# Optimization experiments

Measured on AMD Instinct MI355X. Metric: run time of the kernel, lower is better.

Reference implementation:

```python
import jax, jax.numpy as jnp
from jax import lax
import numpy as np


def _gru_cell(x, h, wih, whh, bih, bhh):
    # torch.nn.GRUCell math: gates split order (r, z, n)
    gi = x @ wih.T + bih          # (N, 3H)
    gh = h @ whh.T + bhh          # (N, 3H)
    ir, iz, i_n = jnp.split(gi, 3, axis=-1)
    hr, hz, h_n = jnp.split(gh, 3, axis=-1)
    r = jax.nn.sigmoid(ir + hr)
    z = jax.nn.sigmoid(iz + hz)
    n = jnp.tanh(i_n + r * h_n)
    return (1.0 - z) * n + z * h


def _dilated_gru(x, dilation, wih, whh, bih, bhh):
    # h_i depends on h_{i-dilation} -> `dilation` independent chains,
    # scanned jointly with a carried state of shape (B*dilation, H).
    B, S, I = x.shape
    H = whh.shape[1]
    nc = S // dilation  # assumes S % dilation == 0
    xr = x.reshape(B, nc, dilation, I).transpose(1, 0, 2, 3).reshape(nc, B * dilation, I)

    def step(h, xt):
        hn = _gru_cell(xt, h, wih, whh, bih, bhh)
        return hn, hn

    h0 = jnp.zeros((B * dilation, H), x.dtype)
    _, ys = lax.scan(step, h0, xr)  # (nc, B*dilation, H)
    return ys.reshape(nc, B, dilation, H).transpose(1, 0, 2, 3).reshape(B, S, H)


def _encoder(data, fparams, bparams, dilations):
    outs = []
    x = data
    for p, d in zip(fparams, dilations):
        x = _dilated_gru(x, d, *p)
        outs.append(x[:, -1, :])
    x = data[:, ::-1, :]
    for p, d in zip(bparams, dilations):
        x = _dilated_gru(x, d, *p)
        outs.append(x[:, -1, :])
    return jnp.concatenate(outs, axis=1)  # (B, 2*sum(hidden_sizes)) = (B, 400)


def setup_inputs() -> dict:
    key = jax.random.key(0)
    ks = jax.random.split(key, 7)
    B, S = 1024, 512
    sizes = [(1, 100), (100, 50), (50, 50)]  # (input_size, hidden_size) per layer

    def cell(k, iS, H):
        k1, k2, k3, k4 = jax.random.split(k, 4)
        s = 1.0 / np.sqrt(H)  # torch GRUCell init: U(-1/sqrt(H), 1/sqrt(H))
        u = lambda kk, shp: jax.random.uniform(kk, shp, jnp.float32, -s, s)
        return u(k1, (3 * H, iS)), u(k2, (3 * H, H)), u(k3, (3 * H,)), u(k4, (3 * H,))

    d = {"data": jax.random.normal(ks[0], (B, S, 1), jnp.float32)}
    for i, nm in enumerate(["f1", "f2", "f3", "b1", "b2", "b3"]):
        iS, H = sizes[i % 3]
        w1, w2, bb1, bb2 = cell(ks[i + 1], iS, H)
        d[nm + "_wih"] = w1
        d[nm + "_whh"] = w2
        d[nm + "_bih"] = bb1
        d[nm + "_bhh"] = bb2
    return d


def reference(data,
              f1_wih, f1_whh, f1_bih, f1_bhh,
              f2_wih, f2_whh, f2_bih, f2_bhh,
              f3_wih, f3_whh, f3_bih, f3_bhh,
              b1_wih, b1_whh, b1_bih, b1_bhh,
              b2_wih, b2_whh, b2_bih, b2_bhh,
              b3_wih, b3_whh, b3_bih, b3_bhh):
    dilations = (1, 4, 16)
    fparams = [(f1_wih, f1_whh, f1_bih, f1_bhh),
               (f2_wih, f2_whh, f2_bih, f2_bhh),
               (f3_wih, f3_whh, f3_bih, f3_bhh)]
    bparams = [(b1_wih, b1_whh, b1_bih, b1_bhh),
               (b2_wih, b2_whh, b2_bih, b2_bhh),
               (b3_wih, b3_whh, b3_bih, b3_bhh)]
    return _encoder(data, fparams, bparams, dilations)
```

## Files before the change

### kernel.cpp

```cpp
#include <hip/hip_runtime.h>
#include <math.h>

typedef short  s16x8 __attribute__((ext_vector_type(8)));
typedef float  f32x4 __attribute__((ext_vector_type(4)));

static __device__ __forceinline__ float sigf(float x){ return 1.0f/(1.0f+__expf(-x)); }
static __device__ __forceinline__ float tanhf_fast(float x){
  float ax=fabsf(x); float e=__expf(-2.0f*ax); float t=(1.0f-e)/(1.0f+e); return copysignf(t,x);
}
static __device__ __forceinline__ unsigned short f2bf(float x){
  unsigned int u = __float_as_uint(x);
  unsigned int r = (u + 0x7FFFu + ((u >> 16) & 1u)) >> 16;
  return (unsigned short)r;
}
static __device__ __forceinline__ float bf2f(unsigned short b){
  return __uint_as_float(((unsigned int)b) << 16);
}
static __device__ __forceinline__ float qsum(float v){
  v += __int_as_float(__builtin_amdgcn_mov_dpp(__float_as_int(v),0xB1,0xF,0xF,true));
  v += __int_as_float(__builtin_amdgcn_mov_dpp(__float_as_int(v),0x4E,0xF,0xF,true));
  return v;
}
static __device__ __forceinline__ float rsum4(float v){
  return v + __int_as_float(__builtin_amdgcn_ds_swizzle(__float_as_int(v), 0x101F));
}
static __device__ __forceinline__ float sel4(int c, float4 v){
  float r=v.x; r=(c==1)?v.y:r; r=(c==2)?v.z:r; r=(c==3)?v.w:r; return r;
}

static __device__ __forceinline__ void load_afrag(const float* __restrict__ whh,
                                                  int gate, int ti, int l, int kc,
                                                  s16x8& hi, s16x8& lo){
  const int r  = ti*16 + (l & 15);
  const int kb = kc*32 + (l >> 4)*8;
  #pragma unroll
  for (int j = 0; j < 8; ++j){
    const int k = kb + j;
    const float wv = (r < 100 && k < 100) ? whh[(size_t)(gate*100 + r)*100 + k] : 0.0f;
    const unsigned short hb = f2bf(wv);
    hi[j] = (short)hb;
    lo[j] = (short)f2bf(wv - bf2f(hb));
  }
}

__global__ __launch_bounds__(448, 2)
void gru_l1(const float* __restrict__ data,
            const float* __restrict__ wih_f, const float* __restrict__ whh_f,
            const float* __restrict__ bih_f, const float* __restrict__ bhh_f,
            const float* __restrict__ wih_b, const float* __restrict__ whh_b,
            const float* __restrict__ bih_b, const float* __restrict__ bhh_b,
            float* __restrict__ x1f, float* __restrict__ x1b,
            float* __restrict__ out)
{
  const int dir   = (int)(blockIdx.x >> 6);
  const int blk16 = (int)(blockIdx.x & 63);
  const int t     = (int)threadIdx.x;
  const float* __restrict__ wih = dir ? wih_b : wih_f;
  const float* __restrict__ whh = dir ? whh_b : whh_f;
  const float* __restrict__ bih = dir ? bih_b : bih_f;
  const float* __restrict__ bhh = dir ? bhh_b : bhh_f;
  float* __restrict__ x1 = dir ? x1b : x1f;
  const int obase = dir ? 200 : 0;
  const int b0 = blk16 * 16;

  __shared__ __align__(16) unsigned short hBhi[2][16][136];
  __shared__ __align__(16) unsigned short hBlo[2][16][136];
  __shared__ __align__(16) float xs[512][16];

  for (int i = t; i < 8192; i += 448){
    const int c  = i >> 9;
    const int sL = i & 511;
    xs[sL][c] = data[(size_t)(b0 + c)*512 + (size_t)(dir ? (511 - sL) : sL)];
  }
  { unsigned short* ph = (unsigned short*)hBhi;
    unsigned short* pl = (unsigned short*)hBlo;
    for (int i = t; i < 2*16*136; i += 448){ ph[i] = 0; pl[i] = 0; } }

  const int l  = t & 63;
  const int W  = t >> 6;

  s16x8 AH00,AH01,AH02,AH03, AH10,AH11,AH12,AH13, AH20,AH21,AH22,AH23;
  s16x8 AL00,AL01,AL02,AL03, AL10,AL11,AL12,AL13, AL20,AL21,AL22,AL23;
  #define LDA(G,KC) load_afrag(whh, G, W, l, KC, AH##G##KC, AL##G##KC);
  LDA(0,0) LDA(0,1) LDA(0,2) LDA(0,3)
  LDA(1,0) LDA(1,1) LDA(1,2) LDA(1,3)
  LDA(2,0) LDA(2,1) LDA(2,2) LDA(2,3)
  #undef LDA

  const int mg  = (l >> 4) * 4;
  const int u0  = W*16 + mg;
  const bool uvalid = (u0 < 100);
  const int u0c = uvalid ? u0 : 96;
  const int c   = l & 15;
  const f32x4 wxr4 = *(const f32x4*)&wih[u0c];
  const f32x4 wxz4 = *(const f32x4*)&wih[100 + u0c];
  const f32x4 wxn4 = *(const f32x4*)&wih[200 + u0c];
  const f32x4 bcr4 = *(const f32x4*)&bih[u0c]       + *(const f32x4*)&bhh[u0c];
  const f32x4 bcz4 = *(const f32x4*)&bih[100 + u0c] + *(const f32x4*)&bhh[100 + u0c];
  const f32x4 bxn4 = *(const f32x4*)&bih[200 + u0c];
  const f32x4 bhn4 = *(const f32x4*)&bhh[200 + u0c];
  f32x4 hprev = {0.f,0.f,0.f,0.f};

  __syncthreads();

  const int bn = l & 15;
  const int bg = (l >> 4)*8;

  #pragma unroll 1
  for (int s = 0; s < 512; ++s){
    const int cur = s & 1, nxt = cur ^ 1;

    const s16x8 BH0 = *(const s16x8*)&hBhi[cur][bn][ 0 + bg];
    const s16x8 BL0 = *(const s16x8*)&hBlo[cur][bn][ 0 + bg];
    const s16x8 BH1 = *(const s16x8*)&hBhi[cur][bn][32 + bg];
    const s16x8 BL1 = *(const s16x8*)&hBlo[cur][bn][32 + bg];
    const s16x8 BH2 = *(const s16x8*)&hBhi[cur][bn][64 + bg];
    const s16x8 BL2 = *(const s16x8*)&hBlo[cur][bn][64 + bg];
    const s16x8 BH3 = *(const s16x8*)&hBhi[cur][bn][96 + bg];
    const s16x8 BL3 = *(const s16x8*)&hBlo[cur][bn][96 + bg];

    f32x4 Ca0={0.f,0.f,0.f,0.f}, Cb0={0.f,0.f,0.f,0.f};
    f32x4 Ca1={0.f,0.f,0.f,0.f}, Cb1={0.f,0.f,0.f,0.f};
    f32x4 Ca2={0.f,0.f,0.f,0.f}, Cb2={0.f,0.f,0.f,0.f};
    #define MM(ACC,G,KC) \
      ACC = __builtin_amdgcn_mfma_f32_16x16x32_bf16(AL##G##KC, BH##KC, ACC, 0, 0, 0); \
      ACC = __builtin_amdgcn_mfma_f32_16x16x32_bf16(AH##G##KC, BL##KC, ACC, 0, 0, 0); \
      ACC = __builtin_amdgcn_mfma_f32_16x16x32_bf16(AH##G##KC, BH##KC, ACC, 0, 0, 0);
    MM(Ca0,0,0) MM(Ca1,1,0) MM(Ca2,2,0)
    MM(Cb0,0,2) MM(Cb1,1,2) MM(Cb2,2,2)
    MM(Ca0,0,1) MM(Ca1,1,1) MM(Ca2,2,1)
    MM(Cb0,0,3) MM(Cb1,1,3) MM(Cb2,2,3)
    #undef MM
    const f32x4 sr = Ca0 + Cb0;
    const f32x4 sz = Ca1 + Cb1;
    const f32x4 sn = Ca2 + Cb2;

    const float xc = xs[s][c];
    f32x4 hn;
    #define FIN(I) { \
      const float rr = sigf(sr[I] + fmaf(wxr4[I], xc, bcr4[I])); \
      const float zz = sigf(sz[I] + fmaf(wxz4[I], xc, bcz4[I])); \
      const float nn = tanhf_fast(fmaf(wxn4[I], xc, bxn4[I]) + rr*(sn[I] + bhn4[I])); \
      hn[I] = nn + zz*(hprev[I] - nn); }
    FIN(0) FIN(1) FIN(2) FIN(3)
    #undef FIN
    hprev = hn;

    if (uvalid){
      const unsigned short h0 = f2bf(hn[0]), h1 = f2bf(hn[1]), h2 = f2bf(hn[2]), h3 = f2bf(hn[3]);
      uint2 vhi, vlo;
      vhi.x = (unsigned int)h0 | ((unsigned int)h1 << 16);
      vhi.y = (unsigned int)h2 | ((unsigned int)h3 << 16);
      vlo.x = (unsigned int)f2bf(hn[0] - bf2f(h0)) | ((unsigned int)f2bf(hn[1] - bf2f(h1)) << 16);
      vlo.y = (unsigned int)f2bf(hn[2] - bf2f(h2)) | ((unsigned int)f2bf(hn[3] - bf2f(h3)) << 16);
      *(uint2*)&hBhi[nxt][c][u0] = vhi;
      *(uint2*)&hBlo[nxt][c][u0] = vlo;
      if ((s & 3) == 3){
        const int cs = s >> 2;
        const int ch = b0 + c;
        const size_t base = (((size_t)cs*256 + (ch >> 2))*100);
        x1[(base + u0 + 0)*4 + (ch & 3)] = hn[0];
        x1[(base + u0 + 1)*4 + (ch & 3)] = hn[1];
        x1[(base + u0 + 2)*4 + (ch & 3)] = hn[2];
        x1[(base + u0 + 3)*4 + (ch & 3)] = hn[3];
      }
      if (s == 511){
        const int ch = b0 + c;
        *(f32x4*)&out[(size_t)ch*400 + obase + u0] = hn;
      }
    }
    __syncthreads();
  }
}

__global__ __launch_bounds__(512, 4)
void gru_l2(const float* __restrict__ x1f, const float* __restrict__ x1b,
            const float* __restrict__ wih_f, const float* __restrict__ whh_f,
            const float* __restrict__ bih_f, const float* __restrict__ bhh_f,
            const float* __restrict__ wih_b, const float* __restrict__ whh_b,
            const float* __restrict__ bih_b, const float* __restrict__ bhh_b,
            float* __restrict__ x2f, float* __restrict__ x2b,
            float* __restrict__ out)
{
  const int dir = (int)(blockIdx.x >> 8);
  const int blk = (int)(blockIdx.x & 255);
  const int t   = (int)threadIdx.x;
  const float* __restrict__ wih = dir ? wih_b : wih_f;
  const float* __restrict__ whh = dir ? whh_b : whh_f;
  const float* __restrict__ bih = dir ? bih_b : bih_f;
  const float* __restrict__ bhh = dir ? bhh_b : bhh_f;
  const float* __restrict__ x1 = dir ? x1b : x1f;
  float* __restrict__ x2 = dir ? x2b : x2f;
  const int obase = dir ? 300 : 100;
  const int b0 = blk * 4;

  __shared__ __align__(16) float xh[2][152][4];

  const int oct = t >> 3;
  const int u   = (oct > 49) ? 49 : oct;
  const int l   = t & 7;
  const int cb  = 19 * l;
  float4 W0,W1,W2,W3,W4,W5,W6,W7,W8,W9,W10,W11,W12,W13,W14,W15,W16,W17,W18;
  #define L2LW(J, V) { const int g = cb + (J); \
    const float wr_ = (g<100) ? wih[(size_t)(u     )*100+g] : ((g<150)? whh[(size_t)(u     )*50+g-100] : 0.f); \
    const float wz_ = (g<100) ? wih[(size_t)(u + 50)*100+g] : ((g<150)? whh[(size_t)(u + 50)*50+g-100] : 0.f); \
    const float wx_ = (g<100) ? wih[(size_t)(u +100)*100+g] : 0.f; \
    const float wh_ = (g>=100 && g<150) ? whh[(size_t)(u +100)*50+g-100] : 0.f; \
    V = make_float4(wr_, wz_, wx_, wh_); }
  L2LW(0,W0)  L2LW(1,W1)  L2LW(2,W2)  L2LW(3,W3)  L2LW(4,W4)  L2LW(5,W5)  L2LW(6,W6)
  L2LW(7,W7)  L2LW(8,W8)  L2LW(9,W9)  L2LW(10,W10) L2LW(11,W11) L2LW(12,W12) L2LW(13,W13)
  L2LW(14,W14) L2LW(15,W15) L2LW(16,W16) L2LW(17,W17) L2LW(18,W18)
  #undef L2LW
  const float bcr = bih[u] + bhh[u];
  const float bcz = bih[u+50] + bhh[u+50];
  const float bxn = bih[u+100];
  const float bhn = bhh[u+100];

  for (int i = t; i < 104; i += 512){
    const int bi = (i >= 52) ? 1 : 0;
    const int row = 100 + (i - bi*52);
    *(float4*)&xh[bi][row][0] = make_float4(0.f,0.f,0.f,0.f);
  }
  if (t < 100)
    *(float4*)&xh[0][t][0] = *(const float4*)(x1 + (((size_t)0*256 + blk)*100 + t)*4);
  __syncthreads();

  #pragma unroll 1
  for (int s = 0; s < 128; ++s){
    const int cur = s & 1, nxt = cur ^ 1;
    if (t < 400){
      const float* hb = &xh[cur][cb][0];
      float ar0=0,ar1=0,ar2=0,ar3=0, az0=0,az1=0,az2=0,az3=0;
      float ax0=0,ax1=0,ax2=0,ax3=0, ah0=0,ah1=0,ah2=0,ah3=0;
      #define L2C(J, WV) { const float4 h4 = *(const float4*)(hb + 4*(J)); \
        ar0=fmaf(WV.x,h4.x,ar0); ar1=fmaf(WV.x,h4.y,ar1); ar2=fmaf(WV.x,h4.z,ar2); ar3=fmaf(WV.x,h4.w,ar3); \
        az0=fmaf(WV.y,h4.x,az0); az1=fmaf(WV.y,h4.y,az1); az2=fmaf(WV.y,h4.z,az2); az3=fmaf(WV.y,h4.w,az3); \
        ax0=fmaf(WV.z,h4.x,ax0); ax1=fmaf(WV.z,h4.y,ax1); ax2=fmaf(WV.z,h4.z,ax2); ax3=fmaf(WV.z,h4.w,ax3); \
        ah0=fmaf(WV.w,h4.x,ah0); ah1=fmaf(WV.w,h4.y,ah1); ah2=fmaf(WV.w,h4.z,ah2); ah3=fmaf(WV.w,h4.w,ah3); }
      L2C(0,W0)  L2C(1,W1)  L2C(2,W2)  L2C(3,W3)  L2C(4,W4)  L2C(5,W5)  L2C(6,W6)
      L2C(7,W7)  L2C(8,W8)  L2C(9,W9)  L2C(10,W10) L2C(11,W11) L2C(12,W12) L2C(13,W13)
      L2C(14,W14) L2C(15,W15) L2C(16,W16) L2C(17,W17) L2C(18,W18)
      #undef L2C
      ar0=qsum(ar0); ar1=qsum(ar1); ar2=qsum(ar2); ar3=qsum(ar3);
      az0=qsum(az0); az1=qsum(az1); az2=qsum(az2); az3=qsum(az3);
      ax0=qsum(ax0); ax1=qsum(ax1); ax2=qsum(ax2); ax3=qsum(ax3);
      ah0=qsum(ah0); ah1=qsum(ah1); ah2=qsum(ah2); ah3=qsum(ah3);
      ar0=rsum4(ar0); ar1=rsum4(ar1); ar2=rsum4(ar2); ar3=rsum4(ar3);
      az0=rsum4(az0); az1=rsum4(az1); az2=rsum4(az2); az3=rsum4(az3);
      ax0=rsum4(ax0); ax1=rsum4(ax1); ax2=rsum4(ax2); ax3=rsum4(ax3);
      ah0=rsum4(ah0); ah1=rsum4(ah1); ah2=rsum4(ah2); ah3=rsum4(ah3);
      if (l < 4){
        const float Ar = sel4(l, make_float4(ar0,ar1,ar2,ar3));
        const float Az = sel4(l, make_float4(az0,az1,az2,az3));
        const float Ax = sel4(l, make_float4(ax0,ax1,ax2,ax3));
        const float Ah = sel4(l, make_float4(ah0,ah1,ah2,ah3));
        const float ho = xh[cur][100+u][l];
        const float r = sigf(Ar + bcr);
        const float z = sigf(Az + bcz);
        const float n = tanhf_fast(Ax + bxn + r*(Ah + bhn));
        const float hnew = n + z*(ho - n);
        xh[nxt][100+u][l] = hnew;
        if ((s & 3) == 3) x2[(((size_t)(s>>2)*256 + blk)*50 + u)*4 + l] = hnew;
        if (s == 127)     out[(size_t)(b0 + l)*400 + obase + u] = hnew;
      }
    } else if (t < 500){
      if (s + 1 < 128){
        const int j = t - 400;
        *(float4*)&xh[nxt][j][0] = *(const float4*)(x1 + (((size_t)(s+1)*256 + blk)*100 + j)*4);
      }
    }
    __syncthreads();
  }
}

__global__ __launch_bounds__(512, 4)
void gru_l3(const float* __restrict__ x2f, const float* __restrict__ x2b,
            const float* __restrict__ wih_f, const float* __restrict__ whh_f,
            const float* __restrict__ bih_f, const float* __restrict__ bhh_f,
            const float* __restrict__ wih_b, const float* __restrict__ whh_b,
            const float* __restrict__ bih_b, const float* __restrict__ bhh_b,
            float* __restrict__ out)
{
  const int dir = (int)(blockIdx.x >> 8);
  const int blk = (int)(blockIdx.x & 255);
  const int t   = (int)threadIdx.x;
  const float* __restrict__ wih = dir ? wih_b : wih_f;
  const float* __restrict__ whh = dir ? whh_b : whh_f;
  const float* __restrict__ bih = dir ? bih_b : bih_f;
  const float* __restrict__ bhh = dir ? bhh_b : bhh_f;
  const float* __restrict__ x2 = dir ? x2b : x2f;
  const int obase = dir ? 350 : 150;
  const int b0 = blk * 4;

  __shared__ __align__(16) float xh[2][104][4];

  const int oct = t >> 3;
  const int u   = (oct > 49) ? 49 : oct;
  const int l   = t & 7;
  const int cb  = 13 * l;
  float4 W0,W1,W2,W3,W4,W5,W6,W7,W8,W9,W10,W11,W12;
  #define L3LW(J, V) { const int g = cb + (J); \
    const float wr_ = (g<50) ? wih[(size_t)(u     )*50+g] : ((g<100)? whh[(size_t)(u     )*50+g-50] : 0.f); \
    const float wz_ = (g<50) ? wih[(size_t)(u + 50)*50+g] : ((g<100)? whh[(size_t)(u + 50)*50+g-50] : 0.f); \
    const float wx_ = (g<50) ? wih[(size_t)(u +100)*50+g] : 0.f; \
    const float wh_ = (g>=50 && g<100) ? whh[(size_t)(u +100)*50+g-50] : 0.f; \
    V = make_float4(wr_, wz_, wx_, wh_); }
  L3LW(0,W0) L3LW(1,W1) L3LW(2,W2) L3LW(3,W3) L3LW(4,W4) L3LW(5,W5) L3LW(6,W6)
  L3LW(7,W7) L3LW(8,W8) L3LW(9,W9) L3LW(10,W10) L3LW(11,W11) L3LW(12,W12)
  #undef L3LW
  const float bcr = bih[u] + bhh[u];
  const float bcz = bih[u+50] + bhh[u+50];
  const float bxn = bih[u+100];
  const float bhn = bhh[u+100];

  for (int i = t; i < 108; i += 512){
    const int bi = (i >= 54) ? 1 : 0;
    const int row = 50 + (i - bi*54);
    *(float4*)&xh[bi][row][0] = make_float4(0.f,0.f,0.f,0.f);
  }
  if (t < 50)
    *(float4*)&xh[0][t][0] = *(const float4*)(x2 + (((size_t)0*256 + blk)*50 + t)*4);
  __syncthreads();

  #pragma unroll 1
  for (int s = 0; s < 32; ++s){
    const int cur = s & 1, nxt = cur ^ 1;
    if (t < 400){
      const float* hb = &xh[cur][cb][0];
      float ar0=0,ar1=0,ar2=0,ar3=0, az0=0,az1=0,az2=0,az3=0;
      float ax0=0,ax1=0,ax2=0,ax3=0, ah0=0,ah1=0,ah2=0,ah3=0;
      #define L3C(J, WV) { const float4 h4 = *(const float4*)(hb + 4*(J)); \
        ar0=fmaf(WV.x,h4.x,ar0); ar1=fmaf(WV.x,h4.y,ar1); ar2=fmaf(WV.x,h4.z,ar2); ar3=fmaf(WV.x,h4.w,ar3); \
        az0=fmaf(WV.y,h4.x,az0); az1=fmaf(WV.y,h4.y,az1); az2=fmaf(WV.y,h4.z,az2); az3=fmaf(WV.y,h4.w,az3); \
        ax0=fmaf(WV.z,h4.x,ax0); ax1=fmaf(WV.z,h4.y,ax1); ax2=fmaf(WV.z,h4.z,ax2); ax3=fmaf(WV.z,h4.w,ax3); \
        ah0=fmaf(WV.w,h4.x,ah0); ah1=fmaf(WV.w,h4.y,ah1); ah2=fmaf(WV.w,h4.z,ah2); ah3=fmaf(WV.w,h4.w,ah3); }
      L3C(0,W0) L3C(1,W1) L3C(2,W2) L3C(3,W3) L3C(4,W4) L3C(5,W5) L3C(6,W6)
      L3C(7,W7) L3C(8,W8) L3C(9,W9) L3C(10,W10) L3C(11,W11) L3C(12,W12)
      #undef L3C
      ar0=qsum(ar0); ar1=qsum(ar1); ar2=qsum(ar2); ar3=qsum(ar3);
      az0=qsum(az0); az1=qsum(az1); az2=qsum(az2); az3=qsum(az3);
      ax0=qsum(ax0); ax1=qsum(ax1); ax2=qsum(ax2); ax3=qsum(ax3);
      ah0=qsum(ah0); ah1=qsum(ah1); ah2=qsum(ah2); ah3=qsum(ah3);
      ar0=rsum4(ar0); ar1=rsum4(ar1); ar2=rsum4(ar2); ar3=rsum4(ar3);
      az0=rsum4(az0); az1=rsum4(az1); az2=rsum4(az2); az3=rsum4(az3);
      ax0=rsum4(ax0); ax1=rsum4(ax1); ax2=rsum4(ax2); ax3=rsum4(ax3);
      ah0=rsum4(ah0); ah1=rsum4(ah1); ah2=rsum4(ah2); ah3=rsum4(ah3);
      if (l < 4){
        const float Ar = sel4(l, make_float4(ar0,ar1,ar2,ar3));
        const float Az = sel4(l, make_float4(az0,az1,az2,az3));
        const float Ax = sel4(l, make_float4(ax0,ax1,ax2,ax3));
        const float Ah = sel4(l, make_float4(ah0,ah1,ah2,ah3));
        const float ho = xh[cur][50+u][l];
        const float r = sigf(Ar + bcr);
        const float z = sigf(Az + bcz);
        const float n = tanhf_fast(Ax + bxn + r*(Ah + bhn));
        const float hnew = n + z*(ho - n);
        xh[nxt][50+u][l] = hnew;
        if (s == 31) out[(size_t)(b0 + l)*400 + obase + u] = hnew;
      }
    } else if (t < 450){
      if (s + 1 < 32){
        const int j = t - 400;
        *(float4*)&xh[nxt][j][0] = *(const float4*)(x2 + (((size_t)(s+1)*256 + blk)*50 + j)*4);
      }
    }
    __syncthreads();
  }
}

extern "C" void kernel_launch(void* const* d_in, const int* in_sizes, int n_in,
                              void* d_out, int out_size, void* d_ws, size_t ws_size,
                              hipStream_t stream)
{
  const float* data   = (const float*)d_in[0];
  const float* f1_wih = (const float*)d_in[1];
  const float* f1_whh = (const float*)d_in[2];
  const float* f1_bih = (const float*)d_in[3];
  const float* f1_bhh = (const float*)d_in[4];
  const float* f2_wih = (const float*)d_in[5];
  const float* f2_whh = (const float*)d_in[6];
  const float* f2_bih = (const float*)d_in[7];
  const float* f2_bhh = (const float*)d_in[8];
  const float* f3_wih = (const float*)d_in[9];
  const float* f3_whh = (const float*)d_in[10];
  const float* f3_bih = (const float*)d_in[11];
  const float* f3_bhh = (const float*)d_in[12];
  const float* b1_wih = (const float*)d_in[13];
  const float* b1_whh = (const float*)d_in[14];
  const float* b1_bih = (const float*)d_in[15];
  const float* b1_bhh = (const float*)d_in[16];
  const float* b2_wih = (const float*)d_in[17];
  const float* b2_whh = (const float*)d_in[18];
  const float* b2_bih = (const float*)d_in[19];
  const float* b2_bhh = (const float*)d_in[20];
  const float* b3_wih = (const float*)d_in[21];
  const float* b3_whh = (const float*)d_in[22];
  const float* b3_bih = (const float*)d_in[23];
  const float* b3_bhh = (const float*)d_in[24];
  float* out = (float*)d_out;

  const size_t X1N = (size_t)128 * 256 * 100 * 4;
  const size_t X2N = (size_t)32 * 256 * 50 * 4;
  if (ws_size < (2 * X1N + 2 * X2N) * sizeof(float)) return;
  float* wsf = (float*)d_ws;
  float* x1f = wsf;
  float* x1b = wsf + X1N;
  float* x2f = wsf + 2 * X1N;
  float* x2b = wsf + 2 * X1N + X2N;

  gru_l1<<<dim3(128), dim3(448), 0, stream>>>(
      data, f1_wih, f1_whh, f1_bih, f1_bhh,
      b1_wih, b1_whh, b1_bih, b1_bhh, x1f, x1b, out);
  gru_l2<<<dim3(512), dim3(512), 0, stream>>>(
      x1f, x1b, f2_wih, f2_whh, f2_bih, f2_bhh,
      b2_wih, b2_whh, b2_bih, b2_bhh, x2f, x2b, out);
  gru_l3<<<dim3(512), dim3(512), 0, stream>>>(
      x2f, x2b, f3_wih, f3_whh, f3_bih, f3_bhh,
      b3_wih, b3_whh, b3_bih, b3_bhh, out);
}
```

Baseline: 1.185 ms.

## Give each wave two hidden tiles in layer-1 GRU, shrink block to four waves

The layer-1 recurrent kernel now runs 4 waves per block, each owning two 16-row output tiles instead of one, so fewer waves join the per-step barrier and more MFMA work runs between barriers. The hidden-state split into bf16 hi/lo now uses the packed v_cvt_pk_bf16_f32 instruction instead of manual rounding. Output pointers are precomputed and advanced per chunk, and the loop is unrolled by two. The cost is roughly double the A-fragment register footprint per thread and a longer serial MFMA chain per wave on the critical recurrence path.

```diff
diff --git a/kernel.cpp b/kernel.cpp
--- a/kernel.cpp
+++ b/kernel.cpp
@@ -16,6 +16,11 @@
 static __device__ __forceinline__ float bf2f(unsigned short b){
   return __uint_as_float(((unsigned int)b) << 16);
 }
+static __device__ __forceinline__ unsigned int cvt_pk_bf16(float a, float b){
+  unsigned int r;
+  asm("v_cvt_pk_bf16_f32 %0, %1, %2" : "=v"(r) : "v"(a), "v"(b));
+  return r;
+}
 static __device__ __forceinline__ float qsum(float v){
   v += __int_as_float(__builtin_amdgcn_mov_dpp(__float_as_int(v),0xB1,0xF,0xF,true));
   v += __int_as_float(__builtin_amdgcn_mov_dpp(__float_as_int(v),0x4E,0xF,0xF,true));
@@ -29,9 +34,9 @@
 }
 
 static __device__ __forceinline__ void load_afrag(const float* __restrict__ whh,
-                                                  int gate, int ti, int l, int kc,
+                                                  int gate, int tile, int l, int kc,
                                                   s16x8& hi, s16x8& lo){
-  const int r  = ti*16 + (l & 15);
+  const int r  = tile*16 + (l & 15);
   const int kb = kc*32 + (l >> 4)*8;
   #pragma unroll
   for (int j = 0; j < 8; ++j){
@@ -43,7 +48,7 @@
   }
 }
 
-__global__ __launch_bounds__(448, 2)
+__global__ __launch_bounds__(256, 1)
 void gru_l1(const float* __restrict__ data,
             const float* __restrict__ wih_f, const float* __restrict__ whh_f,
             const float* __restrict__ bih_f, const float* __restrict__ bhh_f,
@@ -67,48 +72,71 @@
   __shared__ __align__(16) unsigned short hBlo[2][16][136];
   __shared__ __align__(16) float xs[512][16];
 
-  for (int i = t; i < 8192; i += 448){
+  for (int i = t; i < 8192; i += 256){
     const int c  = i >> 9;
     const int sL = i & 511;
     xs[sL][c] = data[(size_t)(b0 + c)*512 + (size_t)(dir ? (511 - sL) : sL)];
   }
   { unsigned short* ph = (unsigned short*)hBhi;
     unsigned short* pl = (unsigned short*)hBlo;
-    for (int i = t; i < 2*16*136; i += 448){ ph[i] = 0; pl[i] = 0; } }
+    for (int i = t; i < 2*16*136; i += 256){ ph[i] = 0; pl[i] = 0; } }
 
   const int l  = t & 63;
   const int W  = t >> 6;
-
-  s16x8 AH00,AH01,AH02,AH03, AH10,AH11,AH12,AH13, AH20,AH21,AH22,AH23;
-  s16x8 AL00,AL01,AL02,AL03, AL10,AL11,AL12,AL13, AL20,AL21,AL22,AL23;
-  #define LDA(G,KC) load_afrag(whh, G, W, l, KC, AH##G##KC, AL##G##KC);
-  LDA(0,0) LDA(0,1) LDA(0,2) LDA(0,3)
-  LDA(1,0) LDA(1,1) LDA(1,2) LDA(1,3)
-  LDA(2,0) LDA(2,1) LDA(2,2) LDA(2,3)
+  const int tA = 2*W, tB = 2*W + 1;
+
+  #define DECLA(G,T) s16x8 AH##G##T##0, AH##G##T##1, AH##G##T##2, AH##G##T##3, \
+                           AL##G##T##0, AL##G##T##1, AL##G##T##2, AL##G##T##3;
+  DECLA(0,a) DECLA(1,a) DECLA(2,a) DECLA(0,b) DECLA(1,b) DECLA(2,b)
+  #undef DECLA
+  #define LDA(G,T,TI) \
+    load_afrag(whh, G, TI, l, 0, AH##G##T##0, AL##G##T##0); \
+    load_afrag(whh, G, TI, l, 1, AH##G##T##1, AL##G##T##1); \
+    load_afrag(whh, G, TI, l, 2, AH##G##T##2, AL##G##T##2); \
+    load_afrag(whh, G, TI, l, 3, AH##G##T##3, AL##G##T##3);
+  LDA(0,a,tA) LDA(1,a,tA) LDA(2,a,tA)
+  LDA(0,b,tB) LDA(1,b,tB) LDA(2,b,tB)
   #undef LDA
 
   const int mg  = (l >> 4) * 4;
-  const int u0  = W*16 + mg;
-  const bool uvalid = (u0 < 100);
-  const int u0c = uvalid ? u0 : 96;
   const int c   = l & 15;
-  const f32x4 wxr4 = *(const f32x4*)&wih[u0c];
-  const f32x4 wxz4 = *(const f32x4*)&wih[100 + u0c];
-  const f32x4 wxn4 = *(const f32x4*)&wih[200 + u0c];
-  const f32x4 bcr4 = *(const f32x4*)&bih[u0c]       + *(const f32x4*)&bhh[u0c];
-  const f32x4 bcz4 = *(const f32x4*)&bih[100 + u0c] + *(const f32x4*)&bhh[100 + u0c];
-  const f32x4 bxn4 = *(const f32x4*)&bih[200 + u0c];
-  const f32x4 bhn4 = *(const f32x4*)&bhh[200 + u0c];
-  f32x4 hprev = {0.f,0.f,0.f,0.f};
+  const int uA0 = tA*16 + mg;
+  const int uB0 = tB*16 + mg;
+  const bool vA = (uA0 < 100);
+  const bool vB = (uB0 < 100);
+  const int uA = vA ? uA0 : 96;
+  const int uB = vB ? uB0 : 96;
+  const f32x4 wxrA = *(const f32x4*)&wih[uA];
+  const f32x4 wxzA = *(const f32x4*)&wih[100 + uA];
+  const f32x4 wxnA = *(const f32x4*)&wih[200 + uA];
+  const f32x4 bcrA = *(const f32x4*)&bih[uA]       + *(const f32x4*)&bhh[uA];
+  const f32x4 bczA = *(const f32x4*)&bih[100 + uA] + *(const f32x4*)&bhh[100 + uA];
+  const f32x4 bxnA = *(const f32x4*)&bih[200 + uA];
+  const f32x4 bhnA = *(const f32x4*)&bhh[200 + uA];
+  const f32x4 wxrB = *(const f32x4*)&wih[uB];
+  const f32x4 wxzB = *(const f32x4*)&wih[100 + uB];
+  const f32x4 wxnB = *(const f32x4*)&wih[200 + uB];
+  const f32x4 bcrB = *(const f32x4*)&bih[uB]       + *(const f32x4*)&bhh[uB];
+  const f32x4 bczB = *(const f32x4*)&bih[100 + uB] + *(const f32x4*)&bhh[100 + uB];
+  const f32x4 bxnB = *(const f32x4*)&bih[200 + uB];
+  const f32x4 bhnB = *(const f32x4*)&bhh[200 + uB];
+  f32x4 hpA = {0.f,0.f,0.f,0.f};
+  f32x4 hpB = {0.f,0.f,0.f,0.f};
+
+  const int ch = b0 + c;
+  float* pA = x1 + ((size_t)(ch >> 2)*100 + uA0)*4 + (ch & 3);
+  float* pB = x1 + ((size_t)(ch >> 2)*100 + uB0)*4 + (ch & 3);
+  const size_t CSSTRIDE = (size_t)256*100*4;
 
   __syncthreads();
 
-  const int bn = l & 15;
+  const int bn = c;
   const int bg = (l >> 4)*8;
 
-  #pragma unroll 1
+  #pragma unroll 2
   for (int s = 0; s < 512; ++s){
     const int cur = s & 1, nxt = cur ^ 1;
+    const float xc = xs[s][c];
 
     const s16x8 BH0 = *(const s16x8*)&hBhi[cur][bn][ 0 + bg];
     const s16x8 BL0 = *(const s16x8*)&hBlo[cur][bn][ 0 + bg];
@@ -119,55 +147,72 @@
     const s16x8 BH3 = *(const s16x8*)&hBhi[cur][bn][96 + bg];
     const s16x8 BL3 = *(const s16x8*)&hBlo[cur][bn][96 + bg];
 
-    f32x4 Ca0={0.f,0.f,0.f,0.f}, Cb0={0.f,0.f,0.f,0.f};
-    f32x4 Ca1={0.f,0.f,0.f,0.f}, Cb1={0.f,0.f,0.f,0.f};
-    f32x4 Ca2={0.f,0.f,0.f,0.f}, Cb2={0.f,0.f,0.f,0.f};
-    #define MM(ACC,G,KC) \
-      ACC = __builtin_amdgcn_mfma_f32_16x16x32_bf16(AL##G##KC, BH##KC, ACC, 0, 0, 0); \
-      ACC = __builtin_amdgcn_mfma_f32_16x16x32_bf16(AH##G##KC, BL##KC, ACC, 0, 0, 0); \
-      ACC = __builtin_amdgcn_mfma_f32_16x16x32_bf16(AH##G##KC, BH##KC, ACC, 0, 0, 0);
-    MM(Ca0,0,0) MM(Ca1,1,0) MM(Ca2,2,0)
-    MM(Cb0,0,2) MM(Cb1,1,2) MM(Cb2,2,2)
-    MM(Ca0,0,1) MM(Ca1,1,1) MM(Ca2,2,1)
-    MM(Cb0,0,3) MM(Cb1,1,3) MM(Cb2,2,3)
-    #undef MM
-    const f32x4 sr = Ca0 + Cb0;
-    const f32x4 sz = Ca1 + Cb1;
-    const f32x4 sn = Ca2 + Cb2;
-
-    const float xc = xs[s][c];
-    f32x4 hn;
-    #define FIN(I) { \
-      const float rr = sigf(sr[I] + fmaf(wxr4[I], xc, bcr4[I])); \
-      const float zz = sigf(sz[I] + fmaf(wxz4[I], xc, bcz4[I])); \
-      const float nn = tanhf_fast(fmaf(wxn4[I], xc, bxn4[I]) + rr*(sn[I] + bhn4[I])); \
-      hn[I] = nn + zz*(hprev[I] - nn); }
-    FIN(0) FIN(1) FIN(2) FIN(3)
+    f32x4 C0a={0.f,0.f,0.f,0.f}, C1a={0.f,0.f,0.f,0.f}, C2a={0.f,0.f,0.f,0.f};
+    f32x4 C0b={0.f,0.f,0.f,0.f}, C1b={0.f,0.f,0.f,0.f}, C2b={0.f,0.f,0.f,0.f};
+    #define MM3(ACC,AH,AL,BH,BL) \
+      ACC = __builtin_amdgcn_mfma_f32_16x16x32_bf16(AL, BH, ACC, 0, 0, 0); \
+      ACC = __builtin_amdgcn_mfma_f32_16x16x32_bf16(AH, BL, ACC, 0, 0, 0); \
+      ACC = __builtin_amdgcn_mfma_f32_16x16x32_bf16(AH, BH, ACC, 0, 0, 0);
+    #define MMKC(KC) \
+      MM3(C0a, AH0a##KC, AL0a##KC, BH##KC, BL##KC) \
+      MM3(C1a, AH1a##KC, AL1a##KC, BH##KC, BL##KC) \
+      MM3(C2a, AH2a##KC, AL2a##KC, BH##KC, BL##KC) \
+      MM3(C0b, AH0b##KC, AL0b##KC, BH##KC, BL##KC) \
+      MM3(C1b, AH1b##KC, AL1b##KC, BH##KC, BL##KC) \
+      MM3(C2b, AH2b##KC, AL2b##KC, BH##KC, BL##KC)
+    MMKC(0) MMKC(1) MMKC(2) MMKC(3)
+    #undef MMKC
+    #undef MM3
+
+    f32x4 hnA, hnB;
+    #define FIN(I,SR,SZ,SN,WXR,WXZ,WXN,BCR,BCZ,BXN,BHN,HP,HN) { \
+      const float rr = sigf(SR[I] + fmaf(WXR[I], xc, BCR[I])); \
+      const float zz = sigf(SZ[I] + fmaf(WXZ[I], xc, BCZ[I])); \
+      const float nn = tanhf_fast(fmaf(WXN[I], xc, BXN[I]) + rr*(SN[I] + BHN[I])); \
+      HN[I] = nn + zz*(HP[I] - nn); }
+    FIN(0,C0a,C1a,C2a,wxrA,wxzA,wxnA,bcrA,bczA,bxnA,bhnA,hpA,hnA)
+    FIN(1,C0a,C1a,C2a,wxrA,wxzA,wxnA,bcrA,bczA,bxnA,bhnA,hpA,hnA)
+    FIN(2,C0a,C1a,C2a,wxrA,wxzA,wxnA,bcrA,bczA,bxnA,bhnA,hpA,hnA)
+    FIN(3,C0a,C1a,C2a,wxrA,wxzA,wxnA,bcrA,bczA,bxnA,bhnA,hpA,hnA)
+    FIN(0,C0b,C1b,C2b,wxrB,wxzB,wxnB,bcrB,bczB,bxnB,bhnB,hpB,hnB)
+    FIN(1,C0b,C1b,C2b,wxrB,wxzB,wxnB,bcrB,bczB,bxnB,bhnB,hpB,hnB)
+    FIN(2,C0b,C1b,C2b,wxrB,wxzB,wxnB,bcrB,bczB,bxnB,bhnB,hpB,hnB)
+    FIN(3,C0b,C1b,C2b,wxrB,wxzB,wxnB,bcrB,bczB,bxnB,bhnB,hpB,hnB)
     #undef FIN
-    hprev = hn;
-
-    if (uvalid){
-      const unsigned short h0 = f2bf(hn[0]), h1 = f2bf(hn[1]), h2 = f2bf(hn[2]), h3 = f2bf(hn[3]);
-      uint2 vhi, vlo;
-      vhi.x = (unsigned int)h0 | ((unsigned int)h1 << 16);
-      vhi.y = (unsigned int)h2 | ((unsigned int)h3 << 16);
-      vlo.x = (unsigned int)f2bf(hn[0] - bf2f(h0)) | ((unsigned int)f2bf(hn[1] - bf2f(h1)) << 16);
-      vlo.y = (unsigned int)f2bf(hn[2] - bf2f(h2)) | ((unsigned int)f2bf(hn[3] - bf2f(h3)) << 16);
-      *(uint2*)&hBhi[nxt][c][u0] = vhi;
-      *(uint2*)&hBlo[nxt][c][u0] = vlo;
-      if ((s & 3) == 3){
-        const int cs = s >> 2;
-        const int ch = b0 + c;
-        const size_t base = (((size_t)cs*256 + (ch >> 2))*100);
-        x1[(base + u0 + 0)*4 + (ch & 3)] = hn[0];
-        x1[(base + u0 + 1)*4 + (ch & 3)] = hn[1];
-        x1[(base + u0 + 2)*4 + (ch & 3)] = hn[2];
-        x1[(base + u0 + 3)*4 + (ch & 3)] = hn[3];
-      }
-      if (s == 511){
-        const int ch = b0 + c;
-        *(f32x4*)&out[(size_t)ch*400 + obase + u0] = hn;
-      }
+    hpA = hnA; hpB = hnB;
+
+    if (vA){
+      const unsigned int px = cvt_pk_bf16(hnA[0], hnA[1]);
+      const unsigned int py = cvt_pk_bf16(hnA[2], hnA[3]);
+      const float l0 = hnA[0] - __uint_as_float(px << 16);
+      const float l1 = hnA[1] - __uint_as_float(px & 0xFFFF0000u);
+      const float l2 = hnA[2] - __uint_as_float(py << 16);
+      const float l3 = hnA[3] - __uint_as_float(py & 0xFFFF0000u);
+      uint2 vhi; vhi.x = px; vhi.y = py;
+      uint2 vlo; vlo.x = cvt_pk_bf16(l0, l1); vlo.y = cvt_pk_bf16(l2, l3);
+      *(uint2*)&hBhi[nxt][c][uA0] = vhi;
+      *(uint2*)&hBlo[nxt][c][uA0] = vlo;
+    }
+    if (vB){
+      const unsigned int px = cvt_pk_bf16(hnB[0], hnB[1]);
+      const unsigned int py = cvt_pk_bf16(hnB[2], hnB[3]);
+      const float l0 = hnB[0] - __uint_as_float(px << 16);
+      const float l1 = hnB[1] - __uint_as_float(px & 0xFFFF0000u);
+      const float l2 = hnB[2] - __uint_as_float(py << 16);
+      const float l3 = hnB[3] - __uint_as_float(py & 0xFFFF0000u);
+      uint2 vhi; vhi.x = px; vhi.y = py;
+      uint2 vlo; vlo.x = cvt_pk_bf16(l0, l1); vlo.y = cvt_pk_bf16(l2, l3);
+      *(uint2*)&hBhi[nxt][c][uB0] = vhi;
+      *(uint2*)&hBlo[nxt][c][uB0] = vlo;
+    }
+
+    if ((s & 3) == 3){
+      if (vA){ pA[0]=hnA[0]; pA[4]=hnA[1]; pA[8]=hnA[2]; pA[12]=hnA[3]; pA += CSSTRIDE; }
+      if (vB){ pB[0]=hnB[0]; pB[4]=hnB[1]; pB[8]=hnB[2]; pB[12]=hnB[3]; pB += CSSTRIDE; }
+    }
+    if (s == 511){
+      if (vA) *(f32x4*)&out[(size_t)ch*400 + obase + uA0] = hnA;
+      if (vB) *(f32x4*)&out[(size_t)ch*400 + obase + uB0] = hnB;
     }
     __syncthreads();
   }
@@ -408,7 +453,7 @@
   float* x2f = wsf + 2 * X1N;
   float* x2b = wsf + 2 * X1N + X2N;
 
-  gru_l1<<<dim3(128), dim3(448), 0, stream>>>(
+  gru_l1<<<dim3(128), dim3(256), 0, stream>>>(
       data, f1_wih, f1_whh, f1_bih, f1_bhh,
       b1_wih, b1_whh, b1_bih, b1_bhh, x1f, x1b, out);
   gru_l2<<<dim3(512), dim3(512), 0, stream>>>(
```

After: 1.223 ms. 3.2% more time.

## Rewrite layer-2 GRU as split-bf16 MFMA kernel over 16-chain tiles

Applied to the files above, without the earlier changes.

Replaces the scalar FMA/DPP-reduction layer-2 recurrence with an MFMA formulation. Each block handles 16 chains, with the concatenated [x;h] vector stored as hi/lo bf16 pairs and weights kept in register A-fragments, mirroring layer 1. It also swaps the manual bf16 rounding for packed v_cvt_pk_bf16 and replaces __syncthreads with a lighter lgkmcnt wait plus s_barrier. The grid shrinks from 512 to 128 blocks, which lowers parallelism and adds padding waste in the K dimension in exchange for matrix-core throughput.

```diff
diff --git a/kernel.cpp b/kernel.cpp
--- a/kernel.cpp
+++ b/kernel.cpp
@@ -16,6 +16,15 @@
 static __device__ __forceinline__ float bf2f(unsigned short b){
   return __uint_as_float(((unsigned int)b) << 16);
 }
+static __device__ __forceinline__ unsigned int cvt_pk_bf16(float a, float b){
+  unsigned int r;
+  asm("v_cvt_pk_bf16_f32 %0, %1, %2" : "=v"(r) : "v"(a), "v"(b));
+  return r;
+}
+static __device__ __forceinline__ void fast_barrier(){
+  asm volatile("s_waitcnt lgkmcnt(0)" ::: "memory");
+  __builtin_amdgcn_s_barrier();
+}
 static __device__ __forceinline__ float qsum(float v){
   v += __int_as_float(__builtin_amdgcn_mov_dpp(__float_as_int(v),0xB1,0xF,0xF,true));
   v += __int_as_float(__builtin_amdgcn_mov_dpp(__float_as_int(v),0x4E,0xF,0xF,true));
@@ -29,9 +38,9 @@
 }
 
 static __device__ __forceinline__ void load_afrag(const float* __restrict__ whh,
-                                                  int gate, int ti, int l, int kc,
+                                                  int gate, int tile, int l, int kc,
                                                   s16x8& hi, s16x8& lo){
-  const int r  = ti*16 + (l & 15);
+  const int r  = tile*16 + (l & 15);
   const int kb = kc*32 + (l >> 4)*8;
   #pragma unroll
   for (int j = 0; j < 8; ++j){
@@ -103,7 +112,7 @@
 
   __syncthreads();
 
-  const int bn = l & 15;
+  const int bn = c;
   const int bg = (l >> 4)*8;
 
   #pragma unroll 1
@@ -147,12 +156,14 @@
     hprev = hn;
 
     if (uvalid){
-      const unsigned short h0 = f2bf(hn[0]), h1 = f2bf(hn[1]), h2 = f2bf(hn[2]), h3 = f2bf(hn[3]);
-      uint2 vhi, vlo;
-      vhi.x = (unsigned int)h0 | ((unsigned int)h1 << 16);
-      vhi.y = (unsigned int)h2 | ((unsigned int)h3 << 16);
-      vlo.x = (unsigned int)f2bf(hn[0] - bf2f(h0)) | ((unsigned int)f2bf(hn[1] - bf2f(h1)) << 16);
-      vlo.y = (unsigned int)f2bf(hn[2] - bf2f(h2)) | ((unsigned int)f2bf(hn[3] - bf2f(h3)) << 16);
+      const unsigned int px = cvt_pk_bf16(hn[0], hn[1]);
+      const unsigned int py = cvt_pk_bf16(hn[2], hn[3]);
+      const float l0 = hn[0] - __uint_as_float(px << 16);
+      const float l1 = hn[1] - __uint_as_float(px & 0xFFFF0000u);
+      const float l2 = hn[2] - __uint_as_float(py << 16);
+      const float l3 = hn[3] - __uint_as_float(py & 0xFFFF0000u);
+      uint2 vhi; vhi.x = px; vhi.y = py;
+      uint2 vlo; vlo.x = cvt_pk_bf16(l0, l1); vlo.y = cvt_pk_bf16(l2, l3);
       *(uint2*)&hBhi[nxt][c][u0] = vhi;
       *(uint2*)&hBlo[nxt][c][u0] = vlo;
       if ((s & 3) == 3){
@@ -169,11 +180,37 @@
         *(f32x4*)&out[(size_t)ch*400 + obase + u0] = hn;
       }
     }
-    __syncthreads();
-  }
-}
-
-__global__ __launch_bounds__(512, 4)
+    fast_barrier();
+  }
+}
+
+static __device__ __forceinline__ float l2w(const float* __restrict__ wih,
+                                            const float* __restrict__ whh,
+                                            int sec, int r, int k){
+  if (r >= 50) return 0.f;
+  if (sec == 2) return (k < 100) ? wih[(size_t)(100 + r)*100 + k] : 0.f;
+  if (sec == 3) return (k >= 104 && k < 154) ? whh[(size_t)(100 + r)*50 + (k - 104)] : 0.f;
+  const int ro = (sec == 1) ? 50 : 0;
+  if (k < 100) return wih[(size_t)(ro + r)*100 + k];
+  if (k >= 104 && k < 154) return whh[(size_t)(ro + r)*50 + (k - 104)];
+  return 0.f;
+}
+static __device__ __forceinline__ void l2_afrag(const float* __restrict__ wih,
+                                                const float* __restrict__ whh,
+                                                int sec, int tile, int l, int kc,
+                                                s16x8& hi, s16x8& lo){
+  const int r  = tile*16 + (l & 15);
+  const int kb = kc*32 + (l >> 4)*8;
+  #pragma unroll
+  for (int j = 0; j < 8; ++j){
+    const float wv = l2w(wih, whh, sec, r, kb + j);
+    const unsigned short hb = f2bf(wv);
+    hi[j] = (short)hb;
+    lo[j] = (short)f2bf(wv - bf2f(hb));
+  }
+}
+
+__global__ __launch_bounds__(256, 1)
 void gru_l2(const float* __restrict__ x1f, const float* __restrict__ x1b,
             const float* __restrict__ wih_f, const float* __restrict__ whh_f,
             const float* __restrict__ bih_f, const float* __restrict__ bhh_f,
@@ -182,9 +219,9 @@
             float* __restrict__ x2f, float* __restrict__ x2b,
             float* __restrict__ out)
 {
-  const int dir = (int)(blockIdx.x >> 8);
-  const int blk = (int)(blockIdx.x & 255);
-  const int t   = (int)threadIdx.x;
+  const int dir   = (int)(blockIdx.x >> 6);
+  const int blk16 = (int)(blockIdx.x & 63);
+  const int t     = (int)threadIdx.x;
   const float* __restrict__ wih = dir ? wih_b : wih_f;
   const float* __restrict__ whh = dir ? whh_b : whh_f;
   const float* __restrict__ bih = dir ? bih_b : bih_f;
@@ -192,84 +229,173 @@
   const float* __restrict__ x1 = dir ? x1b : x1f;
   float* __restrict__ x2 = dir ? x2b : x2f;
   const int obase = dir ? 300 : 100;
-  const int b0 = blk * 4;
-
-  __shared__ __align__(16) float xh[2][152][4];
-
-  const int oct = t >> 3;
-  const int u   = (oct > 49) ? 49 : oct;
-  const int l   = t & 7;
-  const int cb  = 19 * l;
-  float4 W0,W1,W2,W3,W4,W5,W6,W7,W8,W9,W10,W11,W12,W13,W14,W15,W16,W17,W18;
-  #define L2LW(J, V) { const int g = cb + (J); \
-    const float wr_ = (g<100) ? wih[(size_t)(u     )*100+g] : ((g<150)? whh[(size_t)(u     )*50+g-100] : 0.f); \
-    const float wz_ = (g<100) ? wih[(size_t)(u + 50)*100+g] : ((g<150)? whh[(size_t)(u + 50)*50+g-100] : 0.f); \
-    const float wx_ = (g<100) ? wih[(size_t)(u +100)*100+g] : 0.f; \
-    const float wh_ = (g>=100 && g<150) ? whh[(size_t)(u +100)*50+g-100] : 0.f; \
-    V = make_float4(wr_, wz_, wx_, wh_); }
-  L2LW(0,W0)  L2LW(1,W1)  L2LW(2,W2)  L2LW(3,W3)  L2LW(4,W4)  L2LW(5,W5)  L2LW(6,W6)
-  L2LW(7,W7)  L2LW(8,W8)  L2LW(9,W9)  L2LW(10,W10) L2LW(11,W11) L2LW(12,W12) L2LW(13,W13)
-  L2LW(14,W14) L2LW(15,W15) L2LW(16,W16) L2LW(17,W17) L2LW(18,W18)
-  #undef L2LW
-  const float bcr = bih[u] + bhh[u];
-  const float bcz = bih[u+50] + bhh[u+50];
-  const float bxn = bih[u+100];
-  const float bhn = bhh[u+100];
-
-  for (int i = t; i < 104; i += 512){
-    const int bi = (i >= 52) ? 1 : 0;
-    const int row = 100 + (i - bi*52);
-    *(float4*)&xh[bi][row][0] = make_float4(0.f,0.f,0.f,0.f);
-  }
-  if (t < 100)
-    *(float4*)&xh[0][t][0] = *(const float4*)(x1 + (((size_t)0*256 + blk)*100 + t)*4);
+  const int b0 = blk16 * 16;
+
+  __shared__ __align__(16) unsigned short hBhi[2][16][168];
+  __shared__ __align__(16) unsigned short hBlo[2][16][168];
+
+  { unsigned short* ph = (unsigned short*)hBhi;
+    unsigned short* pl = (unsigned short*)hBlo;
+    for (int i = t; i < 2*16*168; i += 256){ ph[i] = 0; pl[i] = 0; } }
+
+  const int l = t & 63;
+  const int W = t >> 6;
+
+  s16x8 AH00,AH01,AH02,AH03,AH04, AH10,AH11,AH12,AH13,AH14,
+        AH20,AH21,AH22,AH23,AH24, AH30,AH31,AH32,AH33,AH34;
+  s16x8 AL00,AL01,AL02,AL03,AL04, AL10,AL11,AL12,AL13,AL14,
+        AL20,AL21,AL22,AL23,AL24, AL30,AL31,AL32,AL33,AL34;
+  #define LDA(SE,KC) l2_afrag(wih, whh, SE, W, l, KC, AH##SE##KC, AL##SE##KC);
+  LDA(0,0) LDA(0,1) LDA(0,2) LDA(0,3) LDA(0,4)
+  LDA(1,0) LDA(1,1) LDA(1,2) LDA(1,3) LDA(1,4)
+  LDA(2,0) LDA(2,1) LDA(2,2) LDA(2,3) LDA(2,4)
+  LDA(3,0) LDA(3,1) LDA(3,2) LDA(3,3) LDA(3,4)
+  #undef LDA
+
+  const int mg = (l >> 4) * 4;
+  const int c  = l & 15;
+  const int u0 = W*16 + mg;
+  const int ch = b0 + c;
+  f32x4 bcr, bcz, bxn, bhn;
+  #pragma unroll
+  for (int i = 0; i < 4; ++i){
+    const int u = (u0 + i < 50) ? (u0 + i) : 49;
+    bcr[i] = bih[u]      + bhh[u];
+    bcz[i] = bih[50 + u] + bhh[50 + u];
+    bxn[i] = bih[100 + u];
+    bhn[i] = bhh[100 + u];
+  }
+  const bool vH = (u0 < 50);
+  f32x4 hp = {0.f,0.f,0.f,0.f};
+
+  float* px = x2 + (((size_t)(ch >> 2))*50 + u0)*4 + (ch & 3);
+  const size_t X2STRIDE = (size_t)256*50*4;
+
+  const int oct  = t >> 4;
+  const int cc   = t & 15;
+  const bool stg = (t < 208);
+  const int u0x  = oct * 8;
+
   __syncthreads();
+
+  if (stg){
+    const float* p = x1 + ((size_t)0*256 + (b0 >> 2) + (cc >> 2))*400 + (cc & 3);
+    float xv[8];
+    #pragma unroll
+    for (int j = 0; j < 8; ++j){
+      const int uu = u0x + j;
+      xv[j] = (uu < 100) ? p[4*uu] : 0.f;
+    }
+    unsigned int h0 = cvt_pk_bf16(xv[0], xv[1]);
+    unsigned int h1 = cvt_pk_bf16(xv[2], xv[3]);
+    unsigned int h2 = cvt_pk_bf16(xv[4], xv[5]);
+    unsigned int h3 = cvt_pk_bf16(xv[6], xv[7]);
+    uint4 vhi; vhi.x=h0; vhi.y=h1; vhi.z=h2; vhi.w=h3;
+    uint4 vlo;
+    vlo.x = cvt_pk_bf16(xv[0]-__uint_as_float(h0<<16), xv[1]-__uint_as_float(h0&0xFFFF0000u));
+    vlo.y = cvt_pk_bf16(xv[2]-__uint_as_float(h1<<16), xv[3]-__uint_as_float(h1&0xFFFF0000u));
+    vlo.z = cvt_pk_bf16(xv[4]-__uint_as_float(h2<<16), xv[5]-__uint_as_float(h2&0xFFFF0000u));
+    vlo.w = cvt_pk_bf16(xv[6]-__uint_as_float(h3<<16), xv[7]-__uint_as_float(h3&0xFFFF0000u));
+    *(uint4*)&hBhi[0][cc][u0x] = vhi;
+    *(uint4*)&hBlo[0][cc][u0x] = vlo;
+  }
+  __syncthreads();
+
+  const int bn = c;
+  const int bg = (l >> 4)*8;
 
   #pragma unroll 1
   for (int s = 0; s < 128; ++s){
     const int cur = s & 1, nxt = cur ^ 1;
-    if (t < 400){
-      const float* hb = &xh[cur][cb][0];
-      float ar0=0,ar1=0,ar2=0,ar3=0, az0=0,az1=0,az2=0,az3=0;
-      float ax0=0,ax1=0,ax2=0,ax3=0, ah0=0,ah1=0,ah2=0,ah3=0;
-      #define L2C(J, WV) { const float4 h4 = *(const float4*)(hb + 4*(J)); \
-        ar0=fmaf(WV.x,h4.x,ar0); ar1=fmaf(WV.x,h4.y,ar1); ar2=fmaf(WV.x,h4.z,ar2); ar3=fmaf(WV.x,h4.w,ar3); \
-        az0=fmaf(WV.y,h4.x,az0); az1=fmaf(WV.y,h4.y,az1); az2=fmaf(WV.y,h4.z,az2); az3=fmaf(WV.y,h4.w,az3); \
-        ax0=fmaf(WV.z,h4.x,ax0); ax1=fmaf(WV.z,h4.y,ax1); ax2=fmaf(WV.z,h4.z,ax2); ax3=fmaf(WV.z,h4.w,ax3); \
-        ah0=fmaf(WV.w,h4.x,ah0); ah1=fmaf(WV.w,h4.y,ah1); ah2=fmaf(WV.w,h4.z,ah2); ah3=fmaf(WV.w,h4.w,ah3); }
-      L2C(0,W0)  L2C(1,W1)  L2C(2,W2)  L2C(3,W3)  L2C(4,W4)  L2C(5,W5)  L2C(6,W6)
-      L2C(7,W7)  L2C(8,W8)  L2C(9,W9)  L2C(10,W10) L2C(11,W11) L2C(12,W12) L2C(13,W13)
-      L2C(14,W14) L2C(15,W15) L2C(16,W16) L2C(17,W17) L2C(18,W18)
-      #undef L2C
-      ar0=qsum(ar0); ar1=qsum(ar1); ar2=qsum(ar2); ar3=qsum(ar3);
-      az0=qsum(az0); az1=qsum(az1); az2=qsum(az2); az3=qsum(az3);
-      ax0=qsum(ax0); ax1=qsum(ax1); ax2=qsum(ax2); ax3=qsum(ax3);
-      ah0=qsum(ah0); ah1=qsum(ah1); ah2=qsum(ah2); ah3=qsum(ah3);
-      ar0=rsum4(ar0); ar1=rsum4(ar1); ar2=rsum4(ar2); ar3=rsum4(ar3);
-      az0=rsum4(az0); az1=rsum4(az1); az2=rsum4(az2); az3=rsum4(az3);
-      ax0=rsum4(ax0); ax1=rsum4(ax1); ax2=rsum4(ax2); ax3=rsum4(ax3);
-      ah0=rsum4(ah0); ah1=rsum4(ah1); ah2=rsum4(ah2); ah3=rsum4(ah3);
-      if (l < 4){
-        const float Ar = sel4(l, make_float4(ar0,ar1,ar2,ar3));
-        const float Az = sel4(l, make_float4(az0,az1,az2,az3));
-        const float Ax = sel4(l, make_float4(ax0,ax1,ax2,ax3));
-        const float Ah = sel4(l, make_float4(ah0,ah1,ah2,ah3));
-        const float ho = xh[cur][100+u][l];
-        const float r = sigf(Ar + bcr);
-        const float z = sigf(Az + bcz);
-        const float n = tanhf_fast(Ax + bxn + r*(Ah + bhn));
-        const float hnew = n + z*(ho - n);
-        xh[nxt][100+u][l] = hnew;
-        if ((s & 3) == 3) x2[(((size_t)(s>>2)*256 + blk)*50 + u)*4 + l] = hnew;
-        if (s == 127)     out[(size_t)(b0 + l)*400 + obase + u] = hnew;
+
+    float xv0=0,xv1=0,xv2=0,xv3=0,xv4=0,xv5=0,xv6=0,xv7=0;
+    if (stg){
+      const int st = (s + 1 < 128) ? (s + 1) : 127;
+      const float* p = x1 + ((size_t)st*256 + (b0 >> 2) + (cc >> 2))*400 + (cc & 3);
+      #define XL(J, V) { const int uu = u0x + (J); \
+        V = (uu < 100) ? p[4*uu] : 0.f; }
+      XL(0,xv0) XL(1,xv1) XL(2,xv2) XL(3,xv3) XL(4,xv4) XL(5,xv5) XL(6,xv6) XL(7,xv7)
+      #undef XL
+    }
+
+    const s16x8 BH0 = *(const s16x8*)&hBhi[cur][bn][  0 + bg];
+    const s16x8 BL0 = *(const s16x8*)&hBlo[cur][bn][  0 + bg];
+    const s16x8 BH1 = *(const s16x8*)&hBhi[cur][bn][ 32 + bg];
+    const s16x8 BL1 = *(const s16x8*)&hBlo[cur][bn][ 32 + bg];
+    const s16x8 BH2 = *(const s16x8*)&hBhi[cur][bn][ 64 + bg];
+    const s16x8 BL2 = *(const s16x8*)&hBlo[cur][bn][ 64 + bg];
+    const s16x8 BH3 = *(const s16x8*)&hBhi[cur][bn][ 96 + bg];
+    const s16x8 BL3 = *(const s16x8*)&hBlo[cur][bn][ 96 + bg];
+    const s16x8 BH4 = *(const s16x8*)&hBhi[cur][bn][128 + bg];
+    const s16x8 BL4 = *(const s16x8*)&hBlo[cur][bn][128 + bg];
+
+    f32x4 CrA={0.f,0.f,0.f,0.f}, CzA={0.f,0.f,0.f,0.f}, CxA={0.f,0.f,0.f,0.f}, ChA={0.f,0.f,0.f,0.f};
+    f32x4 CrB={0.f,0.f,0.f,0.f}, CzB={0.f,0.f,0.f,0.f}, CxB={0.f,0.f,0.f,0.f}, ChB={0.f,0.f,0.f,0.f};
+    #define MF(ACC,A,B) ACC = __builtin_amdgcn_mfma_f32_16x16x32_bf16(A, B, ACC, 0, 0, 0);
+    #define G4(SET,KC,AOP,BOP) \
+      MF(Cr##SET, AOP##0##KC, BOP##KC) MF(Cz##SET, AOP##1##KC, BOP##KC) \
+      MF(Cx##SET, AOP##2##KC, BOP##KC) MF(Ch##SET, AOP##3##KC, BOP##KC)
+    G4(A,0,AL,BH) G4(B,3,AL,BH) G4(A,1,AL,BH) G4(B,4,AL,BH) G4(A,2,AL,BH)
+    G4(A,0,AH,BL) G4(B,3,AH,BL) G4(A,1,AH,BL) G4(B,4,AH,BL) G4(A,2,AH,BL)
+    G4(A,0,AH,BH) G4(B,3,AH,BH) G4(A,1,AH,BH) G4(B,4,AH,BH) G4(A,2,AH,BH)
+    #undef G4
+    #undef MF
+    const f32x4 Cr = CrA + CrB;
+    const f32x4 Cz = CzA + CzB;
+    const f32x4 Cx = CxA + CxB;
+    const f32x4 Ch = ChA + ChB;
+
+    f32x4 hn;
+    #define FIN(I) { \
+      const float rr = sigf(Cr[I] + bcr[I]); \
+      const float zz = sigf(Cz[I] + bcz[I]); \
+      const float nn = tanhf_fast(Cx[I] + bxn[I] + rr*(Ch[I] + bhn[I])); \
+      hn[I] = nn + zz*(hp[I] - nn); }
+    FIN(0) FIN(1) FIN(2) FIN(3)
+    #undef FIN
+    hp = hn;
+
+    if (vH){
+      const unsigned int p0 = cvt_pk_bf16(hn[0], hn[1]);
+      const unsigned int p1 = cvt_pk_bf16(hn[2], hn[3]);
+      const float l0 = hn[0] - __uint_as_float(p0 << 16);
+      const float l1 = hn[1] - __uint_as_float(p0 & 0xFFFF0000u);
+      const float l2 = hn[2] - __uint_as_float(p1 << 16);
+      const float l3 = hn[3] - __uint_as_float(p1 & 0xFFFF0000u);
+      uint2 whi; whi.x = p0; whi.y = p1;
+      uint2 wlo; wlo.x = cvt_pk_bf16(l0, l1); wlo.y = cvt_pk_bf16(l2, l3);
+      *(uint2*)&hBhi[nxt][c][104 + u0] = whi;
+      *(uint2*)&hBlo[nxt][c][104 + u0] = wlo;
+      if ((s & 3) == 3){
+        if (u0 + 0 < 50) px[ 0] = hn[0];
+        if (u0 + 1 < 50) px[ 4] = hn[1];
+        if (u0 + 2 < 50) px[ 8] = hn[2];
+        if (u0 + 3 < 50) px[12] = hn[3];
+        px += X2STRIDE;
       }
-    } else if (t < 500){
-      if (s + 1 < 128){
-        const int j = t - 400;
-        *(float4*)&xh[nxt][j][0] = *(const float4*)(x1 + (((size_t)(s+1)*256 + blk)*100 + j)*4);
+      if (s == 127){
+        if (u0 + 0 < 50) out[(size_t)ch*400 + obase + u0 + 0] = hn[0];
+        if (u0 + 1 < 50) out[(size_t)ch*400 + obase + u0 + 1] = hn[1];
+        if (u0 + 2 < 50) out[(size_t)ch*400 + obase + u0 + 2] = hn[2];
+        if (u0 + 3 < 50) out[(size_t)ch*400 + obase + u0 + 3] = hn[3];
       }
     }
-    __syncthreads();
+
+    if (stg){
+      unsigned int h0 = cvt_pk_bf16(xv0, xv1);
+      unsigned int h1 = cvt_pk_bf16(xv2, xv3);
+      unsigned int h2 = cvt_pk_bf16(xv4, xv5);
+      unsigned int h3 = cvt_pk_bf16(xv6, xv7);
+      uint4 vhi; vhi.x=h0; vhi.y=h1; vhi.z=h2; vhi.w=h3;
+      uint4 vlo;
+      vlo.x = cvt_pk_bf16(xv0-__uint_as_float(h0<<16), xv1-__uint_as_float(h0&0xFFFF0000u));
+      vlo.y = cvt_pk_bf16(xv2-__uint_as_float(h1<<16), xv3-__uint_as_float(h1&0xFFFF0000u));
+      vlo.z = cvt_pk_bf16(xv4-__uint_as_float(h2<<16), xv5-__uint_as_float(h2&0xFFFF0000u));
+      vlo.w = cvt_pk_bf16(xv6-__uint_as_float(h3<<16), xv7-__uint_as_float(h3&0xFFFF0000u));
+      *(uint4*)&hBhi[nxt][cc][u0x] = vhi;
+      *(uint4*)&hBlo[nxt][cc][u0x] = vlo;
+    }
+    fast_barrier();
   }
 }
 
@@ -411,7 +537,7 @@
   gru_l1<<<dim3(128), dim3(448), 0, stream>>>(
       data, f1_wih, f1_whh, f1_bih, f1_bhh,
       b1_wih, b1_whh, b1_bih, b1_bhh, x1f, x1b, out);
-  gru_l2<<<dim3(512), dim3(512), 0, stream>>>(
+  gru_l2<<<dim3(128), dim3(256), 0, stream>>>(
       x1f, x1b, f2_wih, f2_whh, f2_bih, f2_bhh,
       b2_wih, b2_whh, b2_bih, b2_bhh, x2f, x2b, out);
   gru_l3<<<dim3(512), dim3(512), 0, stream>>>(
```

After: 1.024 ms. -13.6%, faster.
